# Performance work log

Measured on AMD Instinct MI355X. Metric: run time of the kernel, lower is better.

Reference implementation:

```python
import jax, jax.numpy as jnp
import numpy as np

N = 262144
FEAT = 64
D = 128
DEPTH = 2
N_LAYERS = 1
SCALE_FEATURES = 0.5
SCALE_STEPS = (1.0 - SCALE_FEATURES) / DEPTH
LN_EPS = 1e-5
SLOPE = 0.01


def leaky(x):
    return jnp.where(x >= 0, x, SLOPE * x)


def layernorm(x):
    mu = x.mean(-1, keepdims=True)
    var = ((x - mu) ** 2).mean(-1, keepdims=True)
    return (x - mu) / jnp.sqrt(var + LN_EPS)


def setup_inputs() -> dict:
    key = jax.random.key(0)
    ks = jax.random.split(key, 12)
    raw_feats = jax.random.normal(ks[0], (N, FEAT), dtype=jnp.float32)
    uids = jnp.arange(N, dtype=jnp.int32)
    id_map = jax.random.randint(ks[1], (N, 1, 2), 0, N, dtype=jnp.int32)
    # FeatureEmbedder params
    slow_mean = jnp.zeros((FEAT,), jnp.float32)
    slow_std = jnp.ones((FEAT,), jnp.float32)
    W_embd = jax.random.normal(ks[2], (FEAT, D), jnp.float32) / np.sqrt(FEAT)
    b_embd = jnp.zeros((D,), jnp.float32)
    Wl = jax.random.normal(ks[3], (N_LAYERS, D, D), jnp.float32) / np.sqrt(D)
    bl = jnp.zeros((N_LAYERS, D), jnp.float32)
    # node_emb params
    W_node = jax.random.normal(ks[4], (D, D), jnp.float32) / np.sqrt(D)
    b_node = jnp.zeros((D,), jnp.float32)
    rezero = jnp.full((1,), 0.1, jnp.float32)  # nonzero so depth loop is active
    W_w = jax.random.normal(ks[5], (D, 1), jnp.float32) * 0.01
    W_v = jax.random.normal(ks[6], (D, 1), jnp.float32) / np.sqrt(D)
    return {
        'raw_feats': raw_feats, 'uids': uids, 'id_map': id_map,
        'slow_mean': slow_mean, 'slow_std': slow_std,
        'W_embd': W_embd, 'b_embd': b_embd, 'Wl': Wl, 'bl': bl,
        'W_node': W_node, 'b_node': b_node, 'rezero': rezero,
        'W_w': W_w, 'W_v': W_v,
    }


def reference(raw_feats, uids, id_map, slow_mean, slow_std, W_embd, b_embd,
              Wl, bl, W_node, b_node, rezero, W_w, W_v):
    # sorted_feats = cat([raw_feats, zeros(1, FEAT)])  -> [N+1, FEAT]
    sorted_feats = jnp.concatenate(
        [raw_feats, jnp.zeros((1, FEAT), raw_feats.dtype)], axis=0)

    # FeatureEmbedder: SlowNorm -> Linear -> leaky, residual blocks, LayerNorm, *scale
    x = (sorted_feats - slow_mean) / (slow_std + 0.001)
    x = leaky(x @ W_embd + b_embd)
    for i in range(N_LAYERS):
        # F.leaky_relu(Sequential(Linear, LeakyReLU)(x)) + x  (double leaky)
        x = leaky(leaky(x @ Wl[i] + bl[i])) + x
    x = layernorm(x) * SCALE_FEATURES  # [N+1, D]

    # uids == arange(N), so uid-value -> row-index lookup is identity
    ids = id_map[:, 0, :]  # [N, 2] row indices into x

    for _ in range(DEPTH):
        feats = x[ids].mean(axis=1)                 # gather [N,2,D] -> mean -> [N,D]
        feats = leaky(feats @ W_node + b_node)       # node_emb
        new = x[:-1] + feats * (SCALE_STEPS * rezero)
        x = jnp.concatenate([new, x[-1:]], axis=0)   # scatter-update rows [:-1]

    x_main = x[:-1]
    w = x_main @ W_w                                  # weight head, no bias
    v = jax.lax.stop_gradient(x_main) @ W_v           # value head on detached x
    return (x_main, w, v)
```

## Files before the change

### kernel.cpp

```cpp
#include <hip/hip_runtime.h>


#define NROWS 262144
#define NBLK  4096

typedef __attribute__((ext_vector_type(8))) short bhalf8;
typedef __attribute__((ext_vector_type(4))) float f32x4;
typedef __attribute__((ext_vector_type(4))) unsigned int u32x4;

__device__ __forceinline__ unsigned short f2bf(float x) {
    union { float f; unsigned u; } v; v.f = x;
    unsigned r = v.u + 0x7FFFu + ((v.u >> 16) & 1u);
    return (unsigned short)(r >> 16);
}
__device__ __forceinline__ float bflo(unsigned u) {
    union { unsigned u; float f; } v; v.u = u << 16; return v.f;
}
__device__ __forceinline__ float bfhi(unsigned u) {
    union { unsigned u; float f; } v; v.u = u & 0xFFFF0000u; return v.f;
}
__device__ __forceinline__ float leaky(float x) { return x >= 0.0f ? x : 0.01f * x; }

__global__ void __launch_bounds__(256)
setup_kernel(const float* __restrict__ smean, const float* __restrict__ sstd,
             const float* __restrict__ Wemb, const float* __restrict__ bemb,
             const float* __restrict__ Wl, const float* __restrict__ Wn,
             unsigned short* __restrict__ wpack, float* __restrict__ bembP)
{
    int task = blockIdx.x * 256 + threadIdx.x;
    if (blockIdx.x < 160) {
        if (task < 8192) {
            int f = task >> 9, idx = task & 511;
            int t = f >> 1, s = f & 1, lane = idx >> 3, j = idx & 7;
            int n = t * 16 + (lane & 15), k = s * 32 + (lane >> 4) * 8 + j;
            wpack[task] = f2bf(Wemb[k * 128 + n] / (sstd[k] + 0.001f));
        } else if (task < 24576) {
            int u = task - 8192;
            int f = u >> 9, idx = u & 511;
            int t = f >> 2, s = f & 3, lane = idx >> 3, j = idx & 7;
            int n = t * 16 + (lane & 15), k = s * 32 + (lane >> 4) * 8 + j;
            wpack[task] = f2bf(Wl[k * 128 + n]);
        } else if (task < 40960) {
            int u = task - 24576;
            int f = u >> 9, idx = u & 511;
            int t = f >> 2, s = f & 3, lane = idx >> 3, j = idx & 7;
            int n = t * 16 + (lane & 15), k = s * 32 + (lane >> 4) * 8 + j;
            wpack[task] = f2bf(0.5f * Wn[k * 128 + n]);
        }
    } else {
        int n = threadIdx.x;
        if (n < 128) {
            float acc = bemb[n];
            for (int k = 0; k < 64; k++)
                acc -= smean[k] / (sstd[k] + 0.001f) * Wemb[k * 128 + n];
            bembP[n] = acc;
        }
    }
}

__global__ void __launch_bounds__(256, 4)
phase_a_kernel(const float* __restrict__ feats,
               const unsigned short* __restrict__ wembF,
               const float* __restrict__ bembP,
               const unsigned short* __restrict__ wlF,
               const float* __restrict__ bl,
               unsigned short* __restrict__ xout)
{
    __shared__ __align__(16) short hb[64 * 136];
    const int tid = threadIdx.x, lane = tid & 63, wv = tid >> 6;
    const int m = lane & 15, q = lane >> 4;
    const int r0 = blockIdx.x * 64;

    const bhalf8* wbe = (const bhalf8*)wembF;
    const bhalf8* wbl = (const bhalf8*)wlF;

    bhalf8 af[2];
    #pragma unroll
    for (int s = 0; s < 2; s++) {
        const float* fp = feats + (size_t)(r0 + wv * 16 + m) * 64 + s * 32 + q * 8;
        f32x4 f0 = __builtin_nontemporal_load((const f32x4*)fp);
        f32x4 f1 = __builtin_nontemporal_load((const f32x4*)(fp + 4));
        bhalf8 a;
        #pragma unroll
        for (int jj = 0; jj < 4; jj++) { a[jj] = (short)f2bf(f0[jj]); a[4 + jj] = (short)f2bf(f1[jj]); }
        af[s] = a;
    }
    f32x4 acc[8] = {};
    #pragma unroll
    for (int s = 0; s < 2; s++)
        #pragma unroll
        for (int t = 0; t < 8; t++)
            acc[t] = __builtin_amdgcn_mfma_f32_16x16x32_bf16(af[s], wbe[(t * 2 + s) * 64 + lane], acc[t], 0, 0, 0);

    unsigned hvp[8][2];
    #pragma unroll
    for (int t = 0; t < 8; t++) {
        float be = bembP[t * 16 + m];
        unsigned short hq[4];
        #pragma unroll
        for (int p = 0; p < 4; p++) {
            float h = leaky(acc[t][p] + be);
            hq[p] = f2bf(h);
            hb[(wv * 16 + q * 4 + p) * 136 + t * 16 + m] = (short)hq[p];
        }
        hvp[t][0] = (unsigned)hq[0] | ((unsigned)hq[1] << 16);
        hvp[t][1] = (unsigned)hq[2] | ((unsigned)hq[3] << 16);
    }
    f32x4 acc2[8] = {};
    #pragma unroll
    for (int s = 0; s < 4; s++) {
        bhalf8 a = *(const bhalf8*)&hb[(wv * 16 + m) * 136 + s * 32 + q * 8];
        #pragma unroll
        for (int t = 0; t < 8; t++)
            acc2[t] = __builtin_amdgcn_mfma_f32_16x16x32_bf16(a, wbl[(t * 4 + s) * 64 + lane], acc2[t], 0, 0, 0);
    }

    float sum[4] = {0, 0, 0, 0}, ssq[4] = {0, 0, 0, 0};
    #pragma unroll
    for (int t = 0; t < 8; t++) {
        float bb = bl[t * 16 + m];
        float h0 = bflo(hvp[t][0]), h1 = bfhi(hvp[t][0]);
        float h2 = bflo(hvp[t][1]), h3 = bfhi(hvp[t][1]);
        float hvv[4] = { h0, h1, h2, h3 };
        #pragma unroll
        for (int p = 0; p < 4; p++) {
            float v = leaky(leaky(acc2[t][p] + bb)) + hvv[p];
            acc2[t][p] = v;
            sum[p] += v; ssq[p] += v * v;
        }
    }
    #pragma unroll
    for (int p = 0; p < 4; p++) {
        #pragma unroll
        for (int d = 1; d < 16; d <<= 1) {
            sum[p] += __shfl_xor(sum[p], d, 64);
            ssq[p] += __shfl_xor(ssq[p], d, 64);
        }
    }
    #pragma unroll
    for (int p = 0; p < 4; p++) {
        float mu  = sum[p] * (1.0f / 128.0f);
        float var = ssq[p] * (1.0f / 128.0f) - mu * mu;
        float rs  = rsqrtf(var + 1e-5f) * 0.5f;
        int row = wv * 16 + q * 4 + p;
        #pragma unroll
        for (int t = 0; t < 8; t++)
            hb[row * 136 + t * 16 + m] = (short)f2bf((acc2[t][p] - mu) * rs);
    }
    __syncthreads();
    for (int c = tid; c < 64 * 16; c += 256) {
        int row = c >> 4, cb = (c & 15) * 8;
        *reinterpret_cast<u32x4*>(&xout[(size_t)(r0 + row) * 128 + cb]) =
            *reinterpret_cast<const u32x4*>(&hb[row * 136 + cb]);
    }
}

template <typename TOUT>
__global__ void __launch_bounds__(256)
prop_kernel(const unsigned short* __restrict__ xin, const int* __restrict__ idmap,
            const unsigned short* __restrict__ wnF, const float* __restrict__ bn,
            const float* __restrict__ rez, const float* __restrict__ Ww,
            const float* __restrict__ Wv, TOUT* __restrict__ xout,
            float* __restrict__ wout, float* __restrict__ vout, int final_pass)
{
    __shared__ __align__(16) short gls[64 * 136];
    const int tid = threadIdx.x, lane = tid & 63, wv = tid >> 6;
    const int m = lane & 15, q = lane >> 4;
    const int crow = tid >> 4, ccb = tid & 15;
    const int r0 = blockIdx.x * 64;
    const bhalf8* wbn = (const bhalf8*)wnF;
    const float scale = 0.25f * rez[0];

    const int myrow = r0 + wv * 16 + m;
    int2 ids = ((const int2*)idmap)[myrow];
    const unsigned short* xa = xin + (size_t)ids.x * 128 + q * 8;
    const unsigned short* xb = xin + (size_t)ids.y * 128 + q * 8;
    u32x4 ga[4], gb[4];
    #pragma unroll
    for (int s = 0; s < 4; s++) {
        ga[s] = __builtin_nontemporal_load((const u32x4*)(xa + s * 32));
        gb[s] = __builtin_nontemporal_load((const u32x4*)(xb + s * 32));
    }

    f32x4 acc[8] = {};
    #pragma unroll
    for (int s = 0; s < 4; s++) {
        bhalf8 a;
        #pragma unroll
        for (int w = 0; w < 4; w++) {
            a[2 * w]     = (short)f2bf(bflo(ga[s][w]) + bflo(gb[s][w]));
            a[2 * w + 1] = (short)f2bf(bfhi(ga[s][w]) + bfhi(gb[s][w]));
        }
        #pragma unroll
        for (int t = 0; t < 8; t++)
            acc[t] = __builtin_amdgcn_mfma_f32_16x16x32_bf16(a, wbn[(t * 4 + s) * 64 + lane], acc[t], 0, 0, 0);
    }

    #pragma unroll
    for (int t = 0; t < 8; t++) {
        float bb = bn[t * 16 + m];
        #pragma unroll
        for (int p = 0; p < 4; p++)
            gls[(wv * 16 + q * 4 + p) * 136 + t * 16 + m] = (short)f2bf(leaky(acc[t][p] + bb) * scale);
    }
    __syncthreads();

    #pragma unroll
    for (int i = 0; i < 4; i++) {
        int row = i * 16 + crow;
        u32x4 gv = *(const u32x4*)&gls[row * 136 + ccb * 8];
        u32x4 xv = __builtin_nontemporal_load(
            (const u32x4*)(xin + (size_t)(r0 + row) * 128 + ccb * 8));
        float xn[8];
        #pragma unroll
        for (int w = 0; w < 4; w++) {
            xn[2 * w]     = bflo(xv[w]) + bflo(gv[w]);
            xn[2 * w + 1] = bfhi(xv[w]) + bfhi(gv[w]);
        }
        if (!final_pass) {
            u32x4 ov;
            #pragma unroll
            for (int w = 0; w < 4; w++)
                ov[w] = (unsigned)f2bf(xn[2 * w]) | ((unsigned)f2bf(xn[2 * w + 1]) << 16);
            *reinterpret_cast<u32x4*>(reinterpret_cast<unsigned short*>(xout) + (size_t)(r0 + row) * 128 + ccb * 8) = ov;
        } else {
            float* op = reinterpret_cast<float*>(xout) + (size_t)(r0 + row) * 128 + ccb * 8;
            f32x4 o0, o1;
            #pragma unroll
            for (int w = 0; w < 4; w++) { o0[w] = xn[w]; o1[w] = xn[4 + w]; }
            *reinterpret_cast<f32x4*>(op)     = o0;
            *reinterpret_cast<f32x4*>(op + 4) = o1;
            f32x4 w0 = *(const f32x4*)&Ww[ccb * 8], w1 = *(const f32x4*)&Ww[ccb * 8 + 4];
            f32x4 v0 = *(const f32x4*)&Wv[ccb * 8], v1 = *(const f32x4*)&Wv[ccb * 8 + 4];
            float ws = 0.0f, vs = 0.0f;
            #pragma unroll
            for (int w = 0; w < 4; w++) {
                ws += xn[w] * w0[w] + xn[4 + w] * w1[w];
                vs += xn[w] * v0[w] + xn[4 + w] * v1[w];
            }
            #pragma unroll
            for (int d = 1; d < 16; d <<= 1) {
                ws += __shfl_xor(ws, d, 64);
                vs += __shfl_xor(vs, d, 64);
            }
            if ((lane & 15) == 0) { wout[r0 + row] = ws; vout[r0 + row] = vs; }
        }
    }
}

extern "C" void kernel_launch(void* const* d_in, const int* in_sizes, int n_in,
                              void* d_out, int out_size, void* d_ws, size_t ws_size,
                              hipStream_t stream) {
    const float* feats = (const float*)d_in[0];
    const int*   idmap = (const int*)d_in[2];
    const float* smean = (const float*)d_in[3];
    const float* sstd  = (const float*)d_in[4];
    const float* Wemb  = (const float*)d_in[5];
    const float* bemb  = (const float*)d_in[6];
    const float* Wl    = (const float*)d_in[7];
    const float* bl    = (const float*)d_in[8];
    const float* Wn    = (const float*)d_in[9];
    const float* bn    = (const float*)d_in[10];
    const float* rez   = (const float*)d_in[11];
    const float* Ww    = (const float*)d_in[12];
    const float* Wv    = (const float*)d_in[13];

    char* ws = (char*)d_ws;
    unsigned short* wpack = (unsigned short*)ws;
    float*          bembP = (float*)(ws + 81920);
    unsigned short* x1    = (unsigned short*)(ws + (1ull << 20));

    float* out = (float*)d_out;
    unsigned short* x0 = (unsigned short*)d_out;
    float* wout = out + (size_t)NROWS * 128;
    float* vout = wout + NROWS;

    setup_kernel<<<161, 256, 0, stream>>>(smean, sstd, Wemb, bemb, Wl, Wn, wpack, bembP);
    phase_a_kernel<<<NBLK, 256, 0, stream>>>(feats, wpack, bembP, wpack + 8192, bl, x0);
    prop_kernel<unsigned short><<<NBLK, 256, 0, stream>>>(x0, idmap, wpack + 24576, bn, rez, Ww, Wv,
                                                          x1, nullptr, nullptr, 0);
    prop_kernel<float><<<NBLK, 256, 0, stream>>>(x1, idmap, wpack + 24576, bn, rez, Ww, Wv,
                                                 out, wout, vout, 1);
}
```

Measured before the change: 399.4 us.

## Process two row tiles per block in final propagation pass and prefetch own rows

The final propagation kernel now handles two 64-row tiles per block with half the grid. Both tiles' gathers and own-row loads are issued up front, and the second tile's matmul runs alongside the first tile's epilogue, to hide gather latency. The own rows are loaded early in both passes, and nontemporal loads become plain loads in phase A and the gathers. The cost is higher register pressure and so possibly lower occupancy, plus extra barriers.

```diff
diff --git a/kernel.cpp b/kernel.cpp
--- a/kernel.cpp
+++ b/kernel.cpp
@@ -3,6 +3,7 @@
 
 #define NROWS 262144
 #define NBLK  4096
+#define GRID2 2048
 
 typedef __attribute__((ext_vector_type(8))) short bhalf8;
 typedef __attribute__((ext_vector_type(4))) float f32x4;
@@ -78,8 +79,8 @@
     #pragma unroll
     for (int s = 0; s < 2; s++) {
         const float* fp = feats + (size_t)(r0 + wv * 16 + m) * 64 + s * 32 + q * 8;
-        f32x4 f0 = __builtin_nontemporal_load((const f32x4*)fp);
-        f32x4 f1 = __builtin_nontemporal_load((const f32x4*)(fp + 4));
+        f32x4 f0 = *(const f32x4*)fp;
+        f32x4 f1 = *(const f32x4*)(fp + 4);
         bhalf8 a;
         #pragma unroll
         for (int jj = 0; jj < 4; jj++) { a[jj] = (short)f2bf(f0[jj]); a[4 + jj] = (short)f2bf(f1[jj]); }
@@ -119,9 +120,7 @@
     #pragma unroll
     for (int t = 0; t < 8; t++) {
         float bb = bl[t * 16 + m];
-        float h0 = bflo(hvp[t][0]), h1 = bfhi(hvp[t][0]);
-        float h2 = bflo(hvp[t][1]), h3 = bfhi(hvp[t][1]);
-        float hvv[4] = { h0, h1, h2, h3 };
+        float hvv[4] = { bflo(hvp[t][0]), bfhi(hvp[t][0]), bflo(hvp[t][1]), bfhi(hvp[t][1]) };
         #pragma unroll
         for (int p = 0; p < 4; p++) {
             float v = leaky(leaky(acc2[t][p] + bb)) + hvv[p];
@@ -155,34 +154,21 @@
     }
 }
 
-template <typename TOUT>
-__global__ void __launch_bounds__(256)
-prop_kernel(const unsigned short* __restrict__ xin, const int* __restrict__ idmap,
-            const unsigned short* __restrict__ wnF, const float* __restrict__ bn,
-            const float* __restrict__ rez, const float* __restrict__ Ww,
-            const float* __restrict__ Wv, TOUT* __restrict__ xout,
-            float* __restrict__ wout, float* __restrict__ vout, int final_pass)
-{
-    __shared__ __align__(16) short gls[64 * 136];
-    const int tid = threadIdx.x, lane = tid & 63, wv = tid >> 6;
-    const int m = lane & 15, q = lane >> 4;
-    const int crow = tid >> 4, ccb = tid & 15;
-    const int r0 = blockIdx.x * 64;
-    const bhalf8* wbn = (const bhalf8*)wnF;
-    const float scale = 0.25f * rez[0];
-
-    const int myrow = r0 + wv * 16 + m;
-    int2 ids = ((const int2*)idmap)[myrow];
+__device__ __forceinline__ void gather_rows(const unsigned short* __restrict__ xin,
+                                            int2 ids, int q, u32x4* ga, u32x4* gb)
+{
     const unsigned short* xa = xin + (size_t)ids.x * 128 + q * 8;
     const unsigned short* xb = xin + (size_t)ids.y * 128 + q * 8;
-    u32x4 ga[4], gb[4];
     #pragma unroll
     for (int s = 0; s < 4; s++) {
-        ga[s] = __builtin_nontemporal_load((const u32x4*)(xa + s * 32));
-        gb[s] = __builtin_nontemporal_load((const u32x4*)(xb + s * 32));
-    }
-
-    f32x4 acc[8] = {};
+        ga[s] = *(const u32x4*)(xa + s * 32);
+        gb[s] = *(const u32x4*)(xb + s * 32);
+    }
+}
+
+__device__ __forceinline__ void node_mm(const u32x4* ga, const u32x4* gb,
+                                        const bhalf8* __restrict__ wbn, int lane, f32x4* acc)
+{
     #pragma unroll
     for (int s = 0; s < 4; s++) {
         bhalf8 a;
@@ -195,7 +181,12 @@
         for (int t = 0; t < 8; t++)
             acc[t] = __builtin_amdgcn_mfma_f32_16x16x32_bf16(a, wbn[(t * 4 + s) * 64 + lane], acc[t], 0, 0, 0);
     }
-
+}
+
+__device__ __forceinline__ void stage_g(short* gls, const f32x4* acc,
+                                        const float* __restrict__ bn, float scale,
+                                        int wv, int q, int m)
+{
     #pragma unroll
     for (int t = 0; t < 8; t++) {
         float bb = bn[t * 16 + m];
@@ -203,14 +194,20 @@
         for (int p = 0; p < 4; p++)
             gls[(wv * 16 + q * 4 + p) * 136 + t * 16 + m] = (short)f2bf(leaky(acc[t][p] + bb) * scale);
     }
-    __syncthreads();
-
+}
+
+template <typename TOUT>
+__device__ __forceinline__ void prop_epilogue(const short* gls, const u32x4* xown, int r0,
+                                              const float* __restrict__ Ww, const float* __restrict__ Wv,
+                                              TOUT* __restrict__ xout, float* __restrict__ wout,
+                                              float* __restrict__ vout, int final_pass,
+                                              int crow, int ccb, int lane)
+{
     #pragma unroll
     for (int i = 0; i < 4; i++) {
         int row = i * 16 + crow;
         u32x4 gv = *(const u32x4*)&gls[row * 136 + ccb * 8];
-        u32x4 xv = __builtin_nontemporal_load(
-            (const u32x4*)(xin + (size_t)(r0 + row) * 128 + ccb * 8));
+        u32x4 xv = xown[i];
         float xn[8];
         #pragma unroll
         for (int w = 0; w < 4; w++) {
@@ -248,6 +245,60 @@
     }
 }
 
+template <typename TOUT, int TILES>
+__global__ void __launch_bounds__(256)
+prop_kernel(const unsigned short* __restrict__ xin, const int* __restrict__ idmap,
+            const unsigned short* __restrict__ wnF, const float* __restrict__ bn,
+            const float* __restrict__ rez, const float* __restrict__ Ww,
+            const float* __restrict__ Wv, TOUT* __restrict__ xout,
+            float* __restrict__ wout, float* __restrict__ vout, int final_pass)
+{
+    __shared__ __align__(16) short gls[64 * 136];
+    const int tid = threadIdx.x, lane = tid & 63, wv = tid >> 6;
+    const int m = lane & 15, q = lane >> 4;
+    const int crow = tid >> 4, ccb = tid & 15;
+    const bhalf8* wbn = (const bhalf8*)wnF;
+    const float scale = 0.25f * rez[0];
+
+    const int r0A = blockIdx.x * 64;
+    int2 idsA = ((const int2*)idmap)[r0A + wv * 16 + m];
+    u32x4 gaA[4], gbA[4], xownA[4];
+    gather_rows(xin, idsA, q, gaA, gbA);
+    #pragma unroll
+    for (int i = 0; i < 4; i++)
+        xownA[i] = *(const u32x4*)(xin + (size_t)(r0A + i * 16 + crow) * 128 + ccb * 8);
+
+    if (TILES == 1) {
+        f32x4 acc[8] = {};
+        node_mm(gaA, gbA, wbn, lane, acc);
+        stage_g(gls, acc, bn, scale, wv, q, m);
+        __syncthreads();
+        prop_epilogue(gls, xownA, r0A, Ww, Wv, xout, wout, vout, final_pass, crow, ccb, lane);
+    } else {
+        const int r0B = (blockIdx.x + GRID2) * 64;
+        int2 idsB = ((const int2*)idmap)[r0B + wv * 16 + m];
+        u32x4 gaB[4], gbB[4], xownB[4];
+        gather_rows(xin, idsB, q, gaB, gbB);
+        #pragma unroll
+        for (int i = 0; i < 4; i++)
+            xownB[i] = *(const u32x4*)(xin + (size_t)(r0B + i * 16 + crow) * 128 + ccb * 8);
+
+        f32x4 accA[8] = {};
+        node_mm(gaA, gbA, wbn, lane, accA);
+        stage_g(gls, accA, bn, scale, wv, q, m);
+        __syncthreads();
+
+        f32x4 accB[8] = {};
+        node_mm(gaB, gbB, wbn, lane, accB);
+        prop_epilogue(gls, xownA, r0A, Ww, Wv, xout, wout, vout, final_pass, crow, ccb, lane);
+        __syncthreads();
+
+        stage_g(gls, accB, bn, scale, wv, q, m);
+        __syncthreads();
+        prop_epilogue(gls, xownB, r0B, Ww, Wv, xout, wout, vout, final_pass, crow, ccb, lane);
+    }
+}
+
 extern "C" void kernel_launch(void* const* d_in, const int* in_sizes, int n_in,
                               void* d_out, int out_size, void* d_ws, size_t ws_size,
                               hipStream_t stream) {
@@ -277,8 +328,8 @@
 
     setup_kernel<<<161, 256, 0, stream>>>(smean, sstd, Wemb, bemb, Wl, Wn, wpack, bembP);
     phase_a_kernel<<<NBLK, 256, 0, stream>>>(feats, wpack, bembP, wpack + 8192, bl, x0);
-    prop_kernel<unsigned short><<<NBLK, 256, 0, stream>>>(x0, idmap, wpack + 24576, bn, rez, Ww, Wv,
-                                                          x1, nullptr, nullptr, 0);
-    prop_kernel<float><<<NBLK, 256, 0, stream>>>(x1, idmap, wpack + 24576, bn, rez, Ww, Wv,
-                                                 out, wout, vout, 1);
-}
+    prop_kernel<unsigned short, 1><<<NBLK, 256, 0, stream>>>(x0, idmap, wpack + 24576, bn, rez, Ww, Wv,
+                                                             x1, nullptr, nullptr, 0);
+    prop_kernel<float, 2><<<GRID2, 256, 0, stream>>>(x1, idmap, wpack + 24576, bn, rez, Ww, Wv,
+                                                     out, wout, vout, 1);
+}
```

Result: faster. 351.4 us (-12.0%).
